# Kernel optimization log

Hardware: AMD Instinct MI355X
Metric: run time of the kernel (lower is better)

Reference implementation:

```python
import jax, jax.numpy as jnp
import numpy as np

NC = 80
REG_MAX = 16
STRIDES = (8.0, 16.0, 32.0)
MAX_DET = 300
IOU_THR = 0.7
CONF_THR = 0.001
NCAND = 1024        # top candidates kept before greedy NMS
MAX_WH = 7680.0     # per-class offset trick (ultralytics max_wh)


def _make_anchors(shapes, strides, offset=0.5):
    pts, strs = [], []
    for (h, w), s in zip(shapes, strides):
        sx = jnp.arange(w, dtype=jnp.float32) + offset
        sy = jnp.arange(h, dtype=jnp.float32) + offset
        gy, gx = jnp.meshgrid(sy, sx, indexing='ij')
        pts.append(jnp.stack((gx, gy), -1).reshape(-1, 2))   # (h*w, 2)
        strs.append(jnp.full((h * w, 1), s, jnp.float32))
    return jnp.concatenate(pts, 0), jnp.concatenate(strs, 0)


def _decode_raw(feats):
    """feats_to_raw_yolov8: DFL decode + anchor transform -> pixel cxcywh + sigmoid cls."""
    B = feats[0].shape[0]
    no = 4 * REG_MAX + NC
    merged = jnp.concatenate([f.reshape(B, no, -1) for f in feats], axis=2)  # (B,no,A)
    dist, cls = merged[:, :4 * REG_MAX], merged[:, 4 * REG_MAX:]
    pd = dist.transpose(0, 2, 1).reshape(B, -1, 4, REG_MAX)                  # (B,A,4,reg_max)
    proj = jnp.arange(REG_MAX, dtype=merged.dtype)
    ltrb = jnp.einsum('bafr,r->baf', jax.nn.softmax(pd, -1), proj)           # (B,A,4)
    anchors, strd = _make_anchors([f.shape[2:] for f in feats], STRIDES)     # (A,2),(A,1)
    lt, rb = ltrb[..., :2], ltrb[..., 2:]
    x1y1 = anchors[None] - lt
    x2y2 = anchors[None] + rb
    cxy = (x1y1 + x2y2) * 0.5
    wh = x2y2 - x1y1
    dbox = jnp.concatenate((cxy, wh), -1) * strd[None]                       # (B,A,4) pixel cxcywh
    return dbox, jax.nn.sigmoid(cls).transpose(0, 2, 1)                      # (B,A,nc)


def _iou_one_vs_many(box, boxes):
    lt = jnp.maximum(box[:2], boxes[:, :2])
    rb = jnp.minimum(box[2:], boxes[:, 2:])
    inter = jnp.prod(jnp.clip(rb - lt, 0.0), -1)
    a1 = jnp.prod(box[2:] - box[:2])
    a2 = jnp.prod(boxes[:, 2:] - boxes[:, :2], -1)
    return inter / (a1 + a2 - inter + 1e-7)


def _nms_image(boxes_cxcywh, scores_cls):
    """conf threshold + per-class greedy NMS + max_det truncation -> (max_det, 6)."""
    conf = scores_cls.max(-1)                                   # (A,)
    cls = jnp.argmax(scores_cls, -1).astype(jnp.float32)        # (A,)
    conf = jnp.where(conf > CONF_THR, conf, 0.0)
    top_conf, idx = jax.lax.top_k(conf, NCAND)                  # candidate pre-selection
    cb = boxes_cxcywh[idx]                                      # (NCAND,4) cxcywh
    ccls = cls[idx]
    xy1 = cb[:, :2] - cb[:, 2:] * 0.5
    xy2 = cb[:, :2] + cb[:, 2:] * 0.5
    bx = jnp.concatenate((xy1, xy2), -1) + (ccls * MAX_WH)[:, None]  # class-offset xyxy

    def step(sc, _):
        j = jnp.argmax(sc)
        s = sc[j]
        sup = _iou_one_vs_many(bx[j], bx) > IOU_THR  # self-IoU=1 kills j as well
        return jnp.where(sup, 0.0, sc), (j, s)

    _, (sel, ss) = jax.lax.scan(step, top_conf, None, length=MAX_DET)
    rows = jnp.concatenate((cb[sel], ss[:, None], ccls[sel][:, None]), -1)  # (max_det,6)
    return jnp.where((ss > CONF_THR)[:, None], rows, 0.0)


def setup_inputs() -> dict:
    key = jax.random.key(0)
    k0, k1, k2 = jax.random.split(key, 3)
    B, no = 32, 4 * REG_MAX + NC
    return {
        'feat0': jax.random.normal(k0, (B, no, 80, 80), jnp.float32),
        'feat1': jax.random.normal(k1, (B, no, 40, 40), jnp.float32),
        'feat2': jax.random.normal(k2, (B, no, 20, 20), jnp.float32),
    }


def reference(feat0, feat1, feat2):
    dbox, ps = _decode_raw([feat0, feat1, feat2])        # (B,A,4), (B,A,nc)
    return jax.vmap(_nms_image)(dbox, ps)                # (B, max_det, 6)
```

## Files before the change

### kernel.cpp

```cpp
#include <hip/hip_runtime.h>
#include <stdint.h>

#define NCLS    80
#define NA_TOT  8400
#define NBATCH  32
#define MAXDET  300
#define SSORT   2048
#define RANKCAP 1536
#define CONFTHR 0.001f
#define TILES_PER_IMG 132

__device__ __forceinline__ float xla_expf(float in) {
  const float exp_hi = 88.3762626647950f;
  const float exp_lo = -88.3762626647949f;
  const float LOG2EF = 1.44269504088896341f;
  const float C1 = 0.693359375f;
  const float C2 = -2.12194440e-4f;
  const float p0 = 1.9875691500E-4f, p1 = 1.3981999507E-3f, p2 = 8.3334519073E-3f;
  const float p3 = 4.1665795894E-2f, p4 = 1.6666665459E-1f, p5 = 5.0000001201E-1f;
  float x = fminf(fmaxf(in, exp_lo), exp_hi);
  float fx = floorf(__fadd_rn(__fmul_rn(x, LOG2EF), 0.5f));
  float tmp = __fmul_rn(C1, fx);
  float z   = __fmul_rn(C2, fx);
  x = __fsub_rn(x, tmp);
  x = __fsub_rn(x, z);
  float y = __fadd_rn(__fmul_rn(x, p0), p1);
  y = __fadd_rn(__fmul_rn(y, x), p2);
  y = __fadd_rn(__fmul_rn(y, x), p3);
  y = __fadd_rn(__fmul_rn(y, x), p4);
  y = __fadd_rn(__fmul_rn(y, x), p5);
  y = __fadd_rn(__fmul_rn(y, __fmul_rn(x, x)), x);
  y = __fadd_rn(1.0f, y);
  int m = (int)fx;
  float s = __uint_as_float((uint32_t)(m + 127) << 23);
  float r = __fmul_rn(y, s);
  return fmaxf(r, in);
}

__device__ __forceinline__ float xla_sigmoid(float v) {
  float e = xla_expf(-v);
  float den = __fadd_rn(1.0f, e);
  return 1.0f / den;
}

__device__ __forceinline__ void gload_lds16(const float* gp, float* lp) {
  __builtin_amdgcn_global_load_lds(
      (const __attribute__((address_space(1))) void*)gp,
      (__attribute__((address_space(3))) void*)lp, 16, 0, 0);
}

__global__ __launch_bounds__(256) void yolo_decode_kernel(
    const float* __restrict__ f0, const float* __restrict__ f1,
    const float* __restrict__ f2,
    float4* __restrict__ oboxes, float* __restrict__ oconf,
    float* __restrict__ oclsf) {
  __shared__ float sm[144 * 64];
  int bx  = blockIdx.x;
  int b   = bx / TILES_PER_IMG;
  int r   = bx - b * TILES_PER_IMG;
  int tid = threadIdx.x;
  int lane = tid & 63;
  int wv   = tid >> 6;

  const float* base; int Alvl, W, a0, lvlbase; float stridef;
  if (r < 100)      { base = f0 + (size_t)b * (144 * 6400); W = 80; Alvl = 6400;
                      a0 = r * 64; stridef = 8.0f; lvlbase = 0; }
  else if (r < 125) { base = f1 + (size_t)b * (144 * 1600); W = 40; Alvl = 1600;
                      a0 = (r - 100) * 64; stridef = 16.0f; lvlbase = 6400; }
  else              { base = f2 + (size_t)b * (144 * 400);  W = 20; Alvl = 400;
                      int aa = (r - 125) * 64; a0 = (aa + 64 <= 400) ? aa : 336;
                      stridef = 32.0f; lvlbase = 8000; }

  #pragma unroll
  for (int qq = 0; qq < 9; ++qq) {
    int chunk = wv * 9 + qq;
    int c     = chunk * 4 + (lane >> 4);
    int s     = (c >> 4) & 3;
    int idx4  = (lane & 15) ^ (s << 2);
    const float* gp = base + (size_t)c * Alvl + a0 + idx4 * 4;
    gload_lds16(gp, sm + chunk * 256);
  }
  asm volatile("s_waitcnt vmcnt(0)" ::: "memory");
  __builtin_amdgcn_s_barrier();

  const float* S = sm;
  int idx = tid >> 2;
  int w   = tid & 3;
  int ai  = a0 + idx;
  float ax = __fadd_rn((float)(ai % W), 0.5f);
  float ay = __fadd_rn((float)(ai / W), 0.5f);

  int sidx = idx ^ (w << 4);
  float d[16];
  float mx = -INFINITY;
  #pragma unroll
  for (int rr = 0; rr < 16; ++rr) {
    d[rr] = S[(w * 16 + rr) * 64 + sidx];
    mx = fmaxf(mx, d[rr]);
  }
  float e[16]; float ssum = 0.0f;
  #pragma unroll
  for (int rr = 0; rr < 16; ++rr) {
    e[rr] = xla_expf(__fsub_rn(d[rr], mx));
    ssum = __fadd_rn(ssum, e[rr]);
  }
  float acc = 0.0f;
  #pragma unroll
  for (int rr = 0; rr < 16; ++rr) {
    float p = e[rr] / ssum;
    acc = __fadd_rn(acc, __fmul_rn(p, (float)rr));
  }

  int l0 = lane & ~3;
  float lt0 = __shfl(acc, l0 + 0);
  float lt1 = __shfl(acc, l0 + 1);
  float lt2 = __shfl(acc, l0 + 2);
  float lt3 = __shfl(acc, l0 + 3);

  float best = -INFINITY, second = -INFINITY; int bi = 0;
  #pragma unroll 5
  for (int kk = 0; kk < 20; ++kk) {
    int c = 64 + w * 20 + kk;
    float v = S[c * 64 + (idx ^ (((c >> 4) & 3) << 4))];
    if (v > best)        { second = best; best = v; bi = w * 20 + kk; }
    else if (v > second) { second = v; }
  }
  float gb = __shfl(best, l0 + 0), gs = __shfl(second, l0 + 0);
  int   gi = __shfl(bi,   l0 + 0);
  #pragma unroll
  for (int qq = 1; qq < 4; ++qq) {
    float bq = __shfl(best, l0 + qq), sq = __shfl(second, l0 + qq);
    int   iq = __shfl(bi,   l0 + qq);
    if (bq > gb) { gs = fmaxf(gb, sq); gb = bq; gi = iq; }
    else         { gs = fmaxf(gs, bq); }
  }

  float conf = 0.0f; int cls = gi;
  if (__fsub_rn(gb, gs) < 1e-4f || gb > 5.0f) {
    if (w == 0) {
      float bs = -INFINITY; int bj = 0;
      for (int kk = 0; kk < NCLS; ++kk) {
        int c = 64 + kk;
        float v = S[c * 64 + (idx ^ (((c >> 4) & 3) << 4))];
        float s2 = xla_sigmoid(v);
        if (s2 > bs) { bs = s2; bj = kk; }
      }
      conf = bs; cls = bj;
    }
  } else {
    conf = xla_sigmoid(gb);
  }

  if (w == 0) {
    float x1 = __fsub_rn(ax, lt0);
    float y1 = __fsub_rn(ay, lt1);
    float x2 = __fadd_rn(ax, lt2);
    float y2 = __fadd_rn(ay, lt3);
    float cx = __fmul_rn(__fadd_rn(x1, x2), 0.5f);
    float cy = __fmul_rn(__fadd_rn(y1, y2), 0.5f);
    float ww = __fsub_rn(x2, x1);
    float hh = __fsub_rn(y2, y1);
    int t = b * NA_TOT + lvlbase + a0 + idx;
    oboxes[t] = make_float4(__fmul_rn(cx, stridef), __fmul_rn(cy, stridef),
                            __fmul_rn(ww, stridef), __fmul_rn(hh, stridef));
    conf = (conf > CONFTHR) ? conf : 0.0f;
    oconf[t] = conf;
    oclsf[t] = (float)cls;
  }
}

struct __align__(16) SelLds {
  union {
    struct {
      unsigned long long sortkeys[SSORT];
      unsigned confL[NA_TOT];
      unsigned hist[16][257];
      unsigned tot[257];
      unsigned Tarr[257];
    } a;
    unsigned long long rows[1024][16];
  } u;
  float    rowdata[1024][6];
  unsigned list[1024];
  unsigned clsCnt[NCLS];
  unsigned clsBase[NCLS];
  unsigned clsCur[NCLS];
  unsigned long long alive[16];
};

__global__ __launch_bounds__(1024) void yolo_selectnms_kernel(
    const float4* __restrict__ boxes, const float* __restrict__ conf,
    const float* __restrict__ clsf, float* __restrict__ out) {
  __shared__ SelLds u;
  __shared__ unsigned s_need, s_prefix, s_found, s_B, s_scnt, s_cut, s_done,
                      s_efinal;
  int b    = blockIdx.x;
  int tid  = threadIdx.x;
  int lane = tid & 63;
  int wv   = tid >> 6;
  const unsigned* confu = (const unsigned*)conf + (size_t)b * NA_TOT;

  for (int i = tid; i < NA_TOT; i += 1024) u.u.a.confL[i] = confu[i];
  #pragma unroll
  for (int q = 0; q < 6; ++q) u.rowdata[tid][q] = 0.0f;
  if (tid < NCLS) u.clsCnt[tid] = 0;
  if (tid < 16)   u.alive[tid]  = 0ull;
  if (tid == 0) { s_need = 1024; s_prefix = 0; s_cut = 0; s_done = 0;
                  s_scnt = 0; s_efinal = 0; }
  __syncthreads();

  for (int lv = 0; lv < 4; ++lv) {
    __syncthreads();
    if (s_done) break;
    for (int i = tid; i < 16 * 257; i += 1024) ((unsigned*)u.u.a.hist)[i] = 0;
    if (tid == 0) { s_found = 0; s_B = 0; }
    __syncthreads();
    unsigned pfx = s_prefix;
    for (int it = 0; it < 9; ++it) {
      int i = tid + it * 1024;
      unsigned c = (i < NA_TOT) ? u.u.a.confL[i] : 0u;
      bool in; unsigned bin;
      if (lv == 0)      { in = true;                bin = c >> 23; }
      else if (lv == 1) { in = ((c >> 23) == pfx);  bin = (c >> 15) & 0xFF; }
      else if (lv == 2) { in = ((c >> 15) == pfx);  bin = (c >> 7) & 0xFF; }
      else              { in = ((c >> 7)  == pfx);  bin = c & 0x7F; }
      bool act = (c != 0) && in;
      unsigned long long ab = __ballot(act);
      if (ab) {
        int fl = __ffsll(ab) - 1;
        unsigned fbin = __shfl(bin, fl);
        unsigned long long same = __ballot(act && (bin == fbin));
        if (same == ab) {
          if (lane == fl) atomicAdd(&u.u.a.hist[wv][fbin], (unsigned)__popcll(ab));
        } else if (act) {
          atomicAdd(&u.u.a.hist[wv][bin], 1u);
        }
      }
    }
    __syncthreads();
    if (tid < 256) {
      unsigned s = 0;
      #pragma unroll
      for (int q = 0; q < 16; ++q) s += u.u.a.hist[q][tid];
      u.u.a.tot[tid] = s;
    }
    __syncthreads();
    if (tid < 64) {
      unsigned carry = 0;
      if (tid == 0) u.u.a.Tarr[256] = 0;
      for (int ch = 3; ch >= 0; --ch) {
        int bb = ch * 64 + tid;
        unsigned v = u.u.a.tot[bb];
        #pragma unroll
        for (int off = 1; off < 64; off <<= 1) {
          unsigned t2 = __shfl_down(v, off);
          if (tid + off < 64) v += t2;
        }
        u.u.a.Tarr[bb] = v + carry;
        carry += __shfl(v, 0);
      }
    }
    __syncthreads();
    unsigned need = s_need;
    if (tid < 256) {
      unsigned h = u.u.a.tot[tid];
      if (h > 0 && u.u.a.Tarr[tid + 1] < need && u.u.a.Tarr[tid + 1] + h >= need) {
        s_B = (unsigned)tid; s_found = 1;
      }
    }
    __syncthreads();
    if (tid == 0) {
      if (!s_found) { s_cut = 1; s_done = 1; }
      else {
        unsigned B = s_B;
        unsigned selcnt = (1024u - need) + u.u.a.Tarr[B];
        if (selcnt <= (unsigned)RANKCAP || lv == 3) {
          s_done = 1;
          if (lv == 0)      s_cut = B << 23;
          else if (lv == 1) s_cut = (s_prefix << 23) | (B << 15);
          else if (lv == 2) s_cut = (s_prefix << 15) | (B << 7);
          else              s_cut = (s_prefix << 7)  | B;
        } else {
          s_need   = need - u.u.a.Tarr[B + 1];
          s_prefix = (s_prefix << 8) | B;
        }
      }
    }
  }
  __syncthreads();

  unsigned cut = s_cut;
  for (int it = 0; it < 9; ++it) {
    int i = tid + it * 1024;
    unsigned c = (i < NA_TOT) ? u.u.a.confL[i] : 0u;
    bool sel = (c != 0 && c >= cut);
    unsigned long long bal = __ballot(sel);
    unsigned base2 = 0;
    if (lane == 0 && bal) base2 = atomicAdd(&s_scnt, (unsigned)__popcll(bal));
    base2 = __shfl(base2, 0);
    if (sel) {
      unsigned p = base2 + (unsigned)__popcll(bal & ((1ull << lane) - 1ull));
      if (p < SSORT)
        u.u.a.sortkeys[p] = ((unsigned long long)c << 32) |
                            (unsigned long long)(0xFFFFFFFFu - (unsigned)i);
    }
  }
  __syncthreads();
  {
    unsigned scnt = s_scnt; if (scnt > SSORT) scnt = SSORT;
    for (unsigned p = scnt + tid; p < SSORT; p += 1024) u.u.a.sortkeys[p] = 0ull;
  }
  __syncthreads();

  for (int k = 2; k <= SSORT; k <<= 1) {
    for (int j = k >> 1; j > 0; j >>= 1) {
      int i = ((tid & ~(j - 1)) << 1) | (tid & (j - 1));
      int l = i | j;
      unsigned long long A = u.u.a.sortkeys[i], Bv = u.u.a.sortkeys[l];
      bool up = ((i & k) == 0);
      if (up ? (A > Bv) : (A < Bv)) { u.u.a.sortkeys[i] = Bv; u.u.a.sortkeys[l] = A; }
      __syncthreads();
    }
  }

  {
    unsigned long long key = u.u.a.sortkeys[SSORT - 1 - tid];
    bool valid = (key >> 32) != 0ull;
    if (valid) {
      unsigned a = 0xFFFFFFFFu - (unsigned)(key & 0xFFFFFFFFull);
      float4 cb = boxes[(size_t)b * NA_TOT + a];
      float cls = clsf[(size_t)b * NA_TOT + a];
      u.rowdata[tid][0] = cb.x;
      u.rowdata[tid][1] = cb.y;
      u.rowdata[tid][2] = cb.z;
      u.rowdata[tid][3] = cb.w;
      u.rowdata[tid][4] = __uint_as_float((unsigned)(key >> 32));
      u.rowdata[tid][5] = cls;
      atomicOr(&u.alive[tid >> 6], 1ull << (tid & 63));
      atomicAdd(&u.clsCnt[(int)cls], 1u);
    }
  }
  __syncthreads();

  #pragma unroll
  for (int q = 0; q < 16; ++q) u.u.rows[tid][q] = 0ull;
  if (tid == 0) {
    unsigned acc = 0;
    for (int c2 = 0; c2 < NCLS; ++c2) {
      u.clsBase[c2] = acc; u.clsCur[c2] = acc; acc += u.clsCnt[c2];
    }
  }
  __syncthreads();
  bool valid = (u.alive[tid >> 6] >> (tid & 63)) & 1ull;
  float mycls = u.rowdata[tid][5];
  if (valid) {
    unsigned p = atomicAdd(&u.clsCur[(int)mycls], 1u);
    u.list[p] = (unsigned)tid;
  }
  __syncthreads();

  if (valid) {
    float bx0 = u.rowdata[tid][0], by0 = u.rowdata[tid][1];
    float bw0 = u.rowdata[tid][2], bh0 = u.rowdata[tid][3];
    int c = (int)mycls;
    unsigned base = u.clsBase[c], cnt = u.clsCnt[c];
    float off = __fmul_rn(mycls, 7680.0f);
    float hw  = __fmul_rn(bw0, 0.5f), hh = __fmul_rn(bh0, 0.5f);
    float wx1 = __fadd_rn(__fsub_rn(bx0, hw), off);
    float wy1 = __fadd_rn(__fsub_rn(by0, hh), off);
    float wx2 = __fadd_rn(__fadd_rn(bx0, hw), off);
    float wy2 = __fadd_rn(__fadd_rn(by0, hh), off);
    float a1  = __fmul_rn(__fsub_rn(wx2, wx1), __fsub_rn(wy2, wy1));
    int sw = tid & 15;
    for (unsigned l = 0; l < cnt; ++l) {
      int j = (int)u.list[base + l];
      float jx = u.rowdata[j][0], jy = u.rowdata[j][1];
      float jw = u.rowdata[j][2], jh = u.rowdata[j][3];
      float jhw = __fmul_rn(jw, 0.5f), jhh = __fmul_rn(jh, 0.5f);
      float jx1 = __fadd_rn(__fsub_rn(jx, jhw), off);
      float jy1 = __fadd_rn(__fsub_rn(jy, jhh), off);
      float jx2 = __fadd_rn(__fadd_rn(jx, jhw), off);
      float jy2 = __fadd_rn(__fadd_rn(jy, jhh), off);
      float ltx = fmaxf(wx1, jx1), lty = fmaxf(wy1, jy1);
      float rbx = fminf(wx2, jx2), rby = fminf(wy2, jy2);
      float iw = fmaxf(__fsub_rn(rbx, ltx), 0.0f);
      float ih = fmaxf(__fsub_rn(rby, lty), 0.0f);
      float inter = __fmul_rn(iw, ih);
      float a2 = __fmul_rn(__fsub_rn(jx2, jx1), __fsub_rn(jy2, jy1));
      float den = __fadd_rn(__fsub_rn(__fadd_rn(a1, a2), inter), 1e-7f);
      float iou = inter / den;
      if (iou > 0.7f)
        u.u.rows[tid][(j >> 6) ^ sw] |= (1ull << (j & 63));
    }
  }
  __syncthreads();

  float* orow = out + (size_t)b * (MAXDET * 6);
  if (tid < 64) {
    unsigned long long am = (lane < 16) ? u.alive[lane] : 0ull;
    int e = 0;
    while (e < MAXDET) {
      unsigned long long bal = __ballot(am != 0ull);
      if (bal == 0ull) break;
      int f    = __ffsll((unsigned long long)bal) - 1;
      int myb  = __ffsll((unsigned long long)am) - 1;
      int bitp = __shfl(myb, f);
      int r    = f * 64 + bitp;
      if (lane < 6) orow[e * 6 + lane] = u.rowdata[r][lane];
      unsigned long long rowv =
          (lane < 16) ? u.u.rows[r][lane ^ (r & 15)] : 0ull;
      am &= ~rowv;
      ++e;
    }
    if (tid == 0) s_efinal = (unsigned)e;
  }
  __syncthreads();

  for (int i = (int)s_efinal * 6 + tid; i < MAXDET * 6; i += 1024)
    orow[i] = 0.0f;
}

extern "C" void kernel_launch(void* const* d_in, const int* in_sizes, int n_in,
                              void* d_out, int out_size, void* d_ws, size_t ws_size,
                              hipStream_t stream) {
  const float* f0 = (const float*)d_in[0];
  const float* f1 = (const float*)d_in[1];
  const float* f2 = (const float*)d_in[2];
  float* out = (float*)d_out;

  char* ws = (char*)d_ws;
  float4* boxes = (float4*)ws;
  float*  conf  = (float*)(ws + (size_t)NBATCH * NA_TOT * 16);
  float*  clsf  = (float*)(ws + (size_t)NBATCH * NA_TOT * 20);

  yolo_decode_kernel<<<NBATCH * TILES_PER_IMG, 256, 0, stream>>>(
      f0, f1, f2, boxes, conf, clsf);
  yolo_selectnms_kernel<<<NBATCH, 1024, 0, stream>>>(boxes, conf, clsf, out);
}
```

Before: 147.5 us.

## Replace bitonic sort of candidates with rank-by-counting placement

Drops the 2048-element shared-memory bitonic sort and its many block-wide barriers. Each thread instead computes the rank of its candidate key by counting how many keys are larger, and places the top-1024 directly into row slots. This costs O(n^2) comparisons per block in exchange for removing about 66 __syncthreads rounds; keys are unique, so ranks are distinct.

```diff
diff --git a/kernel.cpp b/kernel.cpp
--- a/kernel.cpp
+++ b/kernel.cpp
@@ -306,37 +306,31 @@
     }
   }
   __syncthreads();
-  {
-    unsigned scnt = s_scnt; if (scnt > SSORT) scnt = SSORT;
-    for (unsigned p = scnt + tid; p < SSORT; p += 1024) u.u.a.sortkeys[p] = 0ull;
-  }
-  __syncthreads();
-
-  for (int k = 2; k <= SSORT; k <<= 1) {
-    for (int j = k >> 1; j > 0; j >>= 1) {
-      int i = ((tid & ~(j - 1)) << 1) | (tid & (j - 1));
-      int l = i | j;
-      unsigned long long A = u.u.a.sortkeys[i], Bv = u.u.a.sortkeys[l];
-      bool up = ((i & k) == 0);
-      if (up ? (A > Bv) : (A < Bv)) { u.u.a.sortkeys[i] = Bv; u.u.a.sortkeys[l] = A; }
-      __syncthreads();
-    }
-  }
-
-  {
-    unsigned long long key = u.u.a.sortkeys[SSORT - 1 - tid];
-    bool valid = (key >> 32) != 0ull;
-    if (valid) {
-      unsigned a = 0xFFFFFFFFu - (unsigned)(key & 0xFFFFFFFFull);
+  unsigned scnt = s_scnt; if (scnt > SSORT) scnt = SSORT;
+  unsigned snp = (scnt + 1u) & ~1u;
+  if (tid == 0 && (scnt & 1u)) u.u.a.sortkeys[scnt] = 0ull;
+  __syncthreads();
+
+  for (unsigned e = tid; e < scnt; e += 1024) {
+    unsigned long long mykey = u.u.a.sortkeys[e];
+    unsigned r = 0;
+    #pragma unroll 4
+    for (unsigned j = 0; j < snp; j += 2) {
+      ulonglong2 kk = *reinterpret_cast<const ulonglong2*>(&u.u.a.sortkeys[j]);
+      r += (kk.x > mykey) ? 1u : 0u;
+      r += (kk.y > mykey) ? 1u : 0u;
+    }
+    if (r < 1024) {
+      unsigned a = 0xFFFFFFFFu - (unsigned)(mykey & 0xFFFFFFFFull);
       float4 cb = boxes[(size_t)b * NA_TOT + a];
       float cls = clsf[(size_t)b * NA_TOT + a];
-      u.rowdata[tid][0] = cb.x;
-      u.rowdata[tid][1] = cb.y;
-      u.rowdata[tid][2] = cb.z;
-      u.rowdata[tid][3] = cb.w;
-      u.rowdata[tid][4] = __uint_as_float((unsigned)(key >> 32));
-      u.rowdata[tid][5] = cls;
-      atomicOr(&u.alive[tid >> 6], 1ull << (tid & 63));
+      u.rowdata[r][0] = cb.x;
+      u.rowdata[r][1] = cb.y;
+      u.rowdata[r][2] = cb.z;
+      u.rowdata[r][3] = cb.w;
+      u.rowdata[r][4] = __uint_as_float((unsigned)(mykey >> 32));
+      u.rowdata[r][5] = cls;
+      atomicOr(&u.alive[r >> 6], 1ull << (r & 63));
       atomicAdd(&u.clsCnt[(int)cls], 1u);
     }
   }
```

Measured after the change: 154.0 us. 4.4% more time.
